# Kernel optimization log

Measured on AMD Instinct MI355X. Metric: run time of the kernel, lower is better.

## Reference

```python
import jax, jax.numpy as jnp
import numpy as np

EPS = 1e-12  # F.normalize eps

def _l2norm(v, axis):
    n = jnp.sqrt(jnp.sum(v * v, axis=axis, keepdims=True))
    return v / jnp.maximum(n, EPS)

def setup_inputs() -> dict:
    key = jax.random.key(0)
    ks = jax.random.split(key, 4)
    B, N, C, centers = 128, 196, 768, 64
    x = jax.random.normal(ks[0], (B, N, C), dtype=jnp.float32)
    k_c = jax.random.normal(ks[1], (C, centers), dtype=jnp.float32)
    v_c = jax.random.normal(ks[2], (centers, N, N), dtype=jnp.float32)
    proj_w = jax.random.normal(ks[3], (C, C), dtype=jnp.float32) * (C ** -0.5)
    proj_b = jnp.zeros((C,), dtype=jnp.float32)
    return {"x": x, "k_c": k_c, "v_c": v_c, "proj_w": proj_w, "proj_b": proj_b}

def reference(x, k_c, v_c, proj_w, proj_b):
    # x: (B, N, C); k_c: (C, centers); v_c: (centers, N, N)
    C = x.shape[-1]
    scale = C ** -0.5
    q = x.mean(axis=1)                                  # (B, C)
    attn = _l2norm(q, -1) @ _l2norm(k_c, 0)             # (B, centers)
    attn = jax.nn.softmax(attn * scale, axis=-1)        # (B, centers)
    # attention-weighted mixture of basis matrices: (B,centers)x(centers,N*N) GEMM
    v = jnp.einsum('bc,cnm->bnm', attn, v_c)            # (B, N, N)
    out = jnp.einsum('bnm,bmd->bnd', v, x)              # (B, N, C)
    out = out @ proj_w.T + proj_b                        # Linear(dim, dim)
    return out
```

## Files before the change

kernel.cpp:

```cpp
#include <hip/hip_runtime.h>
#include <hip/hip_bf16.h>


#define NB   128
#define NN   196
#define NC   768
#define NCEN 64
#define MPAD 224
#define RPAD 256
#define BGRP 32

using bf16x8 = __attribute__((ext_vector_type(8))) short;
using f32x4  = __attribute__((ext_vector_type(4))) float;

__device__ __forceinline__ void async_copy16(const void* g, void* l) {
    __builtin_amdgcn_global_load_lds((const __attribute__((address_space(1))) void*)g,
                                     (__attribute__((address_space(3))) void*)l, 16, 0, 0);
}

__global__ __launch_bounds__(256)
void convert_x_kernel(const float* __restrict__ x, __hip_bfloat16* __restrict__ x_t,
                      float* __restrict__ q_sum) {
    __shared__ unsigned short lt[64 * 256];
    __shared__ float qred[32][64];
    int b = blockIdx.x, cc = blockIdx.y, t = threadIdx.x;
    int c0 = cc * 64;
    int c8 = t & 7;
    int ms = t >> 3;
    const float* xp = x + (size_t)b * NN * NC + c0 + c8 * 8;
    float s[8] = {};
#pragma unroll
    for (int it = 0; it < 7; ++it) {
        int m = ms + 32 * it;
        union { bf16x8 v; __hip_bfloat16 h[8]; } u;
        u.v = (bf16x8){};
        if (m < NN) {
            float4 v0 = *(const float4*)(xp + (size_t)m * NC);
            float4 v1 = *(const float4*)(xp + (size_t)m * NC + 4);
            u.h[0] = __float2bfloat16(v0.x); s[0] += v0.x;
            u.h[1] = __float2bfloat16(v0.y); s[1] += v0.y;
            u.h[2] = __float2bfloat16(v0.z); s[2] += v0.z;
            u.h[3] = __float2bfloat16(v0.w); s[3] += v0.w;
            u.h[4] = __float2bfloat16(v1.x); s[4] += v1.x;
            u.h[5] = __float2bfloat16(v1.y); s[5] += v1.y;
            u.h[6] = __float2bfloat16(v1.z); s[6] += v1.z;
            u.h[7] = __float2bfloat16(v1.w); s[7] += v1.w;
        }
        int msw = m ^ (c8 << 3);
#pragma unroll
        for (int j = 0; j < 8; ++j)
            lt[(c8 * 8 + j) * 256 + msw] = ((unsigned short*)&u)[j];
    }
#pragma unroll
    for (int j = 0; j < 8; ++j) qred[ms][c8 * 8 + j] = s[j];
    __syncthreads();
    {
        int r = t >> 2, c4 = t & 3;
        int key = (r >> 3) & 7;
        __hip_bfloat16* xtr = x_t + (size_t)b * NC * MPAD + (size_t)(c0 + r) * MPAD;
#pragma unroll
        for (int ic = 0; ic < 7; ++ic) {
            int ch = c4 + 4 * ic;
            bf16x8 vv = *(const bf16x8*)&lt[r * 256 + ((ch ^ key) << 3)];
            *(bf16x8*)(xtr + ch * 8) = vv;
        }
    }
    if (t < 64) {
        float q = 0.f;
#pragma unroll
        for (int ss = 0; ss < 32; ++ss) q += qred[ss][t];
        q_sum[(size_t)b * NC + c0 + t] = q;
    }
}

__global__ __launch_bounds__(256)
void convert_w_kernel(const float* __restrict__ w, __hip_bfloat16* __restrict__ w_bf) {
    int i = (blockIdx.x * 256 + threadIdx.x) * 8;
    if (i >= NC * NC) return;
    float4 v0 = *(const float4*)(w + i);
    float4 v1 = *(const float4*)(w + i + 4);
    union { bf16x8 v; __hip_bfloat16 h[8]; } u;
    u.h[0] = __float2bfloat16(v0.x);
    u.h[1] = __float2bfloat16(v0.y);
    u.h[2] = __float2bfloat16(v0.z);
    u.h[3] = __float2bfloat16(v0.w);
    u.h[4] = __float2bfloat16(v1.x);
    u.h[5] = __float2bfloat16(v1.y);
    u.h[6] = __float2bfloat16(v1.z);
    u.h[7] = __float2bfloat16(v1.w);
    *(bf16x8*)(w_bf + i) = u.v;
}

__global__ __launch_bounds__(256)
void attn_kernel(const float* __restrict__ q_sum, const float* __restrict__ k_c,
                 float* __restrict__ attn) {
    const float SCALE = 0.03608439182435161f;
    int b = blockIdx.x, t = threadIdx.x;
    __shared__ float qs[NC];
    __shared__ float red[256];
    __shared__ float pd[16][NCEN];
    __shared__ float pk[16][NCEN];

    for (int i = t; i < NC; i += 256)
        qs[i] = q_sum[(size_t)b * NC + i] * (1.0f / (float)NN);
    __syncthreads();

    float s = 0.f;
    for (int i = t; i < NC; i += 256) { float v = qs[i]; s += v * v; }
    red[t] = s;
    __syncthreads();
    for (int o = 128; o > 0; o >>= 1) {
        if (t < o) red[t] += red[t + o];
        __syncthreads();
    }
    float qn = sqrtf(red[0]);

    int j4 = (t & 15) * 4;
    int part = t >> 4;
    const float* kp = k_c + j4;
    float d0 = 0.f, d1 = 0.f, d2 = 0.f, d3 = 0.f;
    float e0 = 0.f, e1 = 0.f, e2 = 0.f, e3 = 0.f;
    int c0 = part * 48;
#pragma unroll 8
    for (int c = c0; c < c0 + 48; ++c) {
        float4 kv = *(const float4*)(kp + (size_t)c * NCEN);
        float qv = qs[c];
        d0 += qv * kv.x; d1 += qv * kv.y; d2 += qv * kv.z; d3 += qv * kv.w;
        e0 += kv.x * kv.x; e1 += kv.y * kv.y; e2 += kv.z * kv.z; e3 += kv.w * kv.w;
    }
    pd[part][j4 + 0] = d0; pd[part][j4 + 1] = d1; pd[part][j4 + 2] = d2; pd[part][j4 + 3] = d3;
    pk[part][j4 + 0] = e0; pk[part][j4 + 1] = e1; pk[part][j4 + 2] = e2; pk[part][j4 + 3] = e3;
    __syncthreads();

    if (t < NCEN) {
        float dot = 0.f, kk = 0.f;
#pragma unroll
        for (int p = 0; p < 16; ++p) { dot += pd[p][t]; kk += pk[p][t]; }
        float kn = sqrtf(kk);
        float lg = dot / (fmaxf(qn, 1e-12f) * fmaxf(kn, 1e-12f)) * SCALE;
        float mx = lg;
        for (int o = 32; o > 0; o >>= 1) mx = fmaxf(mx, __shfl_xor(mx, o, 64));
        float e = expf(lg - mx);
        float sum = e;
        for (int o = 32; o > 0; o >>= 1) sum += __shfl_xor(sum, o, 64);
        attn[b * NCEN + t] = e / sum;
    }
}

__global__ __launch_bounds__(256)
void mix_kernel(const float* __restrict__ attn, const float* __restrict__ v_c,
                __hip_bfloat16* __restrict__ v_pad) {
    int n = blockIdx.x;
    int g = blockIdx.y;
    int m = threadIdx.x;

    __shared__ float sattn[BGRP][NCEN];
    for (int i = threadIdx.x; i < BGRP * NCEN; i += 256)
        sattn[i >> 6][i & 63] = attn[(g * BGRP + (i >> 6)) * NCEN + (i & 63)];
    __syncthreads();

    if (m >= MPAD) return;
    __hip_bfloat16 z = __float2bfloat16(0.f);
    size_t base = (size_t)n * MPAD + m;
    if (n >= NN || m >= NN) {
#pragma unroll
        for (int bb = 0; bb < BGRP; ++bb)
            v_pad[(size_t)(g * BGRP + bb) * RPAD * MPAD + base] = z;
        return;
    }
    float vc[NCEN];
    const float* vp = v_c + (size_t)n * NN + m;
#pragma unroll
    for (int c = 0; c < NCEN; ++c) vc[c] = vp[(size_t)c * NN * NN];
#pragma unroll
    for (int bb = 0; bb < BGRP; ++bb) {
        float acc = 0.f;
#pragma unroll
        for (int c = 0; c < NCEN; ++c) acc += sattn[bb][c] * vc[c];
        v_pad[(size_t)(g * BGRP + bb) * RPAD * MPAD + base] = __float2bfloat16(acc);
    }
}

template <int BK, int OUTMODE, int NBM, int NBN>
__global__ __launch_bounds__(256)
void gemm_nt(const __hip_bfloat16* __restrict__ A, size_t strideA,
             const __hip_bfloat16* __restrict__ Bm, size_t strideB,
             void* __restrict__ Cout, size_t strideC,
             const float* __restrict__ bias,
             int lda, int ldb, int ldc, int K, int Mstore) {
    constexpr int MPG = NBM * NBN;
    int L = blockIdx.x;
    int w = (L & 7) * ((int)gridDim.x >> 3) + (L >> 3);
    int bb = w / MPG;
    int i5 = w - bb * MPG;
    int bm = i5 / NBN, bn = i5 % NBN;

    const unsigned short* Ab = (const unsigned short*)A + (size_t)bb * strideA + (size_t)bm * 128 * lda;
    const unsigned short* Bb = (const unsigned short*)Bm + (size_t)bb * strideB + (size_t)bn * 128 * ldb;

    __shared__ __align__(16) unsigned short sA[128 * BK];
    __shared__ __align__(16) unsigned short sB[128 * BK];

    int tid = threadIdx.x;
    int wave = tid >> 6, lane = tid & 63;
    int wr = wave >> 1, wc = wave & 1;
    int lrow = lane & 15, quad = lane >> 4;

    constexpr int CH  = BK / 8;
    constexpr int RPI = 64 / CH;
    constexpr int NI  = 32 / RPI;
    int srow = lane / CH;
    int sc   = lane % CH;
    int lc   = (BK == 64) ? (sc ^ (srow & 7)) : sc;

    const unsigned short* ga[NI];
    const unsigned short* gb[NI];
    unsigned short* la[NI];
    unsigned short* lb[NI];
#pragma unroll
    for (int i = 0; i < NI; ++i) {
        int row = wave * 32 + i * RPI + srow;
        ga[i] = Ab + (size_t)row * lda + lc * 8;
        gb[i] = Bb + (size_t)row * ldb + lc * 8;
        la[i] = &sA[(wave * 32 + i * RPI) * BK];
        lb[i] = &sB[(wave * 32 + i * RPI) * BK];
    }

    f32x4 acc[4][4] = {};

    for (int k0 = 0; k0 < K; k0 += BK) {
        __syncthreads();
#pragma unroll
        for (int i = 0; i < NI; ++i) async_copy16(ga[i] + k0, la[i]);
#pragma unroll
        for (int i = 0; i < NI; ++i) async_copy16(gb[i] + k0, lb[i]);
        __syncthreads();

#pragma unroll
        for (int kh = 0; kh < BK / 32; ++kh) {
            int pcbase = (BK == 64) ? ((kh * 4 + quad) ^ (lrow & 7)) : quad;
            bf16x8 af[4], bfr[4];
#pragma unroll
            for (int i = 0; i < 4; ++i)
                af[i] = *(const bf16x8*)(&sA[(wr * 64 + i * 16 + lrow) * BK + pcbase * 8]);
#pragma unroll
            for (int j = 0; j < 4; ++j)
                bfr[j] = *(const bf16x8*)(&sB[(wc * 64 + j * 16 + lrow) * BK + pcbase * 8]);
#pragma unroll
            for (int i = 0; i < 4; ++i)
#pragma unroll
                for (int j = 0; j < 4; ++j)
                    acc[i][j] = __builtin_amdgcn_mfma_f32_16x16x32_bf16(af[i], bfr[j], acc[i][j], 0, 0, 0);
        }
    }

    size_t cbase = (size_t)bb * strideC;
#pragma unroll
    for (int i = 0; i < 4; ++i) {
        int row0 = bm * 128 + wr * 64 + i * 16 + quad * 4;
#pragma unroll
        for (int j = 0; j < 4; ++j) {
            int col = bn * 128 + wc * 64 + j * 16 + lrow;
            float badd = (OUTMODE == 0 && bias) ? bias[col] : 0.f;
#pragma unroll
            for (int r2 = 0; r2 < 4; ++r2) {
                int row = row0 + r2;
                if (OUTMODE == 1) {
                    if (row < Mstore) {
                        ((__hip_bfloat16*)Cout)[cbase + (size_t)row * ldc + col] =
                            __float2bfloat16(acc[i][j][r2]);
                    }
                } else {
                    int b2 = row / MPAD;
                    int n  = row - b2 * MPAD;
                    if (n < NN) {
                        ((float*)Cout)[((size_t)b2 * NN + n) * ldc + col] =
                            acc[i][j][r2] + badd;
                    }
                }
            }
        }
    }
}

extern "C" void kernel_launch(void* const* d_in, const int* in_sizes, int n_in,
                              void* d_out, int out_size, void* d_ws, size_t ws_size,
                              hipStream_t stream) {
    const float* x      = (const float*)d_in[0];
    const float* k_c    = (const float*)d_in[1];
    const float* v_c    = (const float*)d_in[2];
    const float* proj_w = (const float*)d_in[3];
    const float* proj_b = (const float*)d_in[4];
    float* out = (float*)d_out;

    char* ws = (char*)d_ws;
    size_t off = 0;
    auto alloc = [&](size_t bytes) {
        void* p = ws + off;
        off = (off + bytes + 255) & ~(size_t)255;
        return p;
    };
    __hip_bfloat16* x_t   = (__hip_bfloat16*)alloc((size_t)NB * NC * MPAD * 2);
    __hip_bfloat16* w_bf  = (__hip_bfloat16*)alloc((size_t)NC * NC * 2);
    __hip_bfloat16* tmp   = (__hip_bfloat16*)alloc((size_t)NB * MPAD * NC * 2);
    __hip_bfloat16* v_pad = (__hip_bfloat16*)alloc((size_t)NB * RPAD * MPAD * 2);
    float* q_sum = (float*)alloc((size_t)NB * NC * 4);
    float* attn  = (float*)alloc((size_t)NB * NCEN * 4);

    convert_x_kernel<<<dim3(NB, 12), 256, 0, stream>>>(x, x_t, q_sum);
    convert_w_kernel<<<dim3((NC * NC / 8 + 255) / 256), 256, 0, stream>>>(proj_w, w_bf);
    attn_kernel<<<dim3(NB), 256, 0, stream>>>(q_sum, k_c, attn);
    mix_kernel<<<dim3(RPAD, NB / BGRP), 256, 0, stream>>>(attn, v_c, v_pad);

    gemm_nt<32, 1, 2, 6><<<dim3(2 * 6 * NB), 256, 0, stream>>>(
        v_pad, (size_t)RPAD * MPAD, x_t, (size_t)NC * MPAD, tmp, (size_t)MPAD * NC,
        nullptr, MPAD, MPAD, NC, MPAD, MPAD);

    gemm_nt<64, 0, 224, 6><<<dim3(224 * 6), 256, 0, stream>>>(
        tmp, 0, w_bf, 0, out, 0,
        proj_b, NC, NC, NC, NC, 224 * NB);
}
```

Before: 264.8 us.

## Replace projection GEMM with 256x256-tile 8-wave double-buffered kernel

```diff
diff --git a/kernel.cpp b/kernel.cpp
--- a/kernel.cpp
+++ b/kernel.cpp
@@ -283,6 +283,116 @@
     }
 }
 
+
+#define STAGE_HALF(ISB, D, H, TS) do {                                         \
+    const unsigned short* gp_ = (ISB) ? gB : gA;                               \
+    size_t go_ = (size_t)((H) * 128) * 768 + (size_t)(TS) * 64;                \
+    unsigned short* lp_ = &lds[((ISB) ? 32768 : 0) + (D) * 16384 + (H) * 8192 + wid * 512]; \
+    async_copy16(gp_ + go_, lp_);                                              \
+    async_copy16(gp_ + go_ + (size_t)64 * 768, lp_ + 4096);                    \
+} while (0)
+
+#define PHASE8(D, MF, FIRST, TS, SISB, SH, VM) do {                            \
+    if (FIRST) {                                                               \
+        _Pragma("unroll")                                                      \
+        for (int n_ = 0; n_ < 4; ++n_) {                                       \
+            bfr[n_][0] = *(const bf16x8*)(&lds[32768 + (D) * 16384 + bRbase + n_ * 1024 + ck0]); \
+            bfr[n_][1] = *(const bf16x8*)(&lds[32768 + (D) * 16384 + bRbase + n_ * 1024 + ck1]); \
+        }                                                                      \
+    }                                                                          \
+    bf16x8 af0_[2], af1_[2];                                                   \
+    _Pragma("unroll")                                                          \
+    for (int m_ = 0; m_ < 2; ++m_) {                                           \
+        af0_[m_] = *(const bf16x8*)(&lds[(D) * 16384 + aRbase + ((MF) + m_) * 1024 + ck0]); \
+        af1_[m_] = *(const bf16x8*)(&lds[(D) * 16384 + aRbase + ((MF) + m_) * 1024 + ck1]); \
+    }                                                                          \
+    if ((TS) < TK) STAGE_HALF(SISB, (D) ^ 1, SH, TS);                          \
+    __builtin_amdgcn_sched_barrier(0);                                         \
+    __builtin_amdgcn_s_barrier();                                              \
+    asm volatile("s_waitcnt lgkmcnt(0)" ::: "memory");                         \
+    __builtin_amdgcn_sched_barrier(0);                                         \
+    __builtin_amdgcn_s_setprio(1);                                             \
+    _Pragma("unroll")                                                          \
+    for (int m_ = 0; m_ < 2; ++m_)                                             \
+        _Pragma("unroll")                                                      \
+        for (int n_ = 0; n_ < 4; ++n_) {                                       \
+            acc[(MF) + m_][n_] = __builtin_amdgcn_mfma_f32_16x16x32_bf16(af0_[m_], bfr[n_][0], acc[(MF) + m_][n_], 0, 0, 0); \
+            acc[(MF) + m_][n_] = __builtin_amdgcn_mfma_f32_16x16x32_bf16(af1_[m_], bfr[n_][1], acc[(MF) + m_][n_], 0, 0, 0); \
+        }                                                                      \
+    __builtin_amdgcn_s_setprio(0);                                             \
+    __builtin_amdgcn_sched_barrier(0);                                         \
+    if (VM) asm volatile("s_waitcnt vmcnt(0)" ::: "memory");                   \
+    __builtin_amdgcn_s_barrier();                                              \
+} while (0)
+
+template <int TK>
+__global__ __launch_bounds__(512, 2)
+void gemm_b8(const __hip_bfloat16* __restrict__ A, const __hip_bfloat16* __restrict__ Bm,
+             float* __restrict__ Cout, const float* __restrict__ bias) {
+    __shared__ __align__(16) unsigned short lds[65536];
+
+    int L = blockIdx.x;
+    int w = (L & 7) * 42 + (L >> 3);
+    int bm = w / 3, bn = w % 3;
+
+    int tid = threadIdx.x;
+    int wid = tid >> 6, lane = tid & 63;
+    int lrow = lane & 15, quad = lane >> 4;
+    int wr = wid >> 2, wcn = wid & 3;
+
+    int srow_lo = wid * 8 + (lane >> 3);
+    int g = ((lane & 7) ^ ((lane >> 3) & 7)) * 8;
+    const unsigned short* gA = (const unsigned short*)A + (size_t)(bm * 256 + srow_lo) * 768 + g;
+    const unsigned short* gB = (const unsigned short*)Bm + (size_t)(bn * 256 + srow_lo) * 768 + g;
+
+    int key = lrow & 7;
+    int ck0 = ((0 + quad) ^ key) * 8;
+    int ck1 = ((4 + quad) ^ key) * 8;
+    int aRbase = (wr * 128 + lrow) * 64;
+    int bRbase = (wcn * 64 + lrow) * 64;
+
+    f32x4 acc[8][4] = {};
+    bf16x8 bfr[4][2];
+
+    STAGE_HALF(0, 0, 0, 0);
+    STAGE_HALF(0, 0, 1, 0);
+    STAGE_HALF(1, 0, 0, 0);
+    STAGE_HALF(1, 0, 1, 0);
+    asm volatile("s_waitcnt vmcnt(0)" ::: "memory");
+    __builtin_amdgcn_s_barrier();
+
+#pragma unroll 1
+    for (int i = 0; i < TK / 2; ++i) {
+        int T = 2 * i;
+        PHASE8(0, 0, true,  T + 1, 0, 0, false);
+        PHASE8(0, 2, false, T + 1, 0, 1, false);
+        PHASE8(0, 4, false, T + 1, 1, 0, false);
+        PHASE8(0, 6, false, T + 1, 1, 1, true);
+        PHASE8(1, 0, true,  T + 2, 0, 0, false);
+        PHASE8(1, 2, false, T + 2, 0, 1, false);
+        PHASE8(1, 4, false, T + 2, 1, 0, false);
+        PHASE8(1, 6, false, T + 2, 1, 1, true);
+    }
+
+#pragma unroll
+    for (int mrep = 0; mrep < 8; ++mrep) {
+        int row0 = bm * 256 + wr * 128 + mrep * 16 + quad * 4;
+#pragma unroll
+        for (int nrep = 0; nrep < 4; ++nrep) {
+            int col = bn * 256 + wcn * 64 + nrep * 16 + lrow;
+            float badd = bias[col];
+#pragma unroll
+            for (int r = 0; r < 4; ++r) {
+                int row = row0 + r;
+                int b2 = row / MPAD;
+                int n  = row - b2 * MPAD;
+                if (n < NN)
+                    Cout[((size_t)b2 * NN + n) * NC + col] = acc[mrep][nrep][r] + badd;
+            }
+        }
+    }
+}
+
 extern "C" void kernel_launch(void* const* d_in, const int* in_sizes, int n_in,
                               void* d_out, int out_size, void* d_ws, size_t ws_size,
                               hipStream_t stream) {
@@ -316,7 +426,5 @@
         v_pad, (size_t)RPAD * MPAD, x_t, (size_t)NC * MPAD, tmp, (size_t)MPAD * NC,
         nullptr, MPAD, MPAD, NC, MPAD, MPAD);
 
-    gemm_nt<64, 0, 224, 6><<<dim3(224 * 6), 256, 0, stream>>>(
-        tmp, 0, w_bf, 0, out, 0,
-        proj_b, NC, NC, NC, NC, 224 * NB);
-}
+    gemm_b8<12><<<dim3(336), 512, 0, stream>>>(tmp, w_bf, out, proj_b);
+}
```

New measurement: 272.3 us. +2.8%, slower.
